# Kernel optimization log

Hardware: AMD Instinct MI355X
Metric: run time of the kernel (lower is better)

## Reference

```python
import jax, jax.numpy as jnp
import numpy as np

B, S, D = 32, 576, 768
G = 24  # sqrt(S)
TEMP = 0.01


def grid_sample_bilinear_zeros(img, grid):
    # img: (B,C,H,W), grid: (B,Hg,Wg,2) in [-1,1]; torch F.grid_sample,
    # mode='bilinear', padding_mode='zeros', align_corners=False
    Bn, C, H, W = img.shape
    gx, gy = grid[..., 0], grid[..., 1]
    ix = ((gx + 1.0) * W - 1.0) * 0.5
    iy = ((gy + 1.0) * H - 1.0) * 0.5
    x0 = jnp.floor(ix); y0 = jnp.floor(iy)
    x1 = x0 + 1.0;      y1 = y0 + 1.0
    wx1 = ix - x0; wx0 = 1.0 - wx1
    wy1 = iy - y0; wy0 = 1.0 - wy1

    def gather(xi, yi):
        valid = (xi >= 0) & (xi <= W - 1) & (yi >= 0) & (yi <= H - 1)
        xc = jnp.clip(xi, 0, W - 1).astype(jnp.int32)
        yc = jnp.clip(yi, 0, H - 1).astype(jnp.int32)
        vals = jax.vmap(lambda im, y, x: im[:, y, x])(img, yc, xc)  # (B,C,Hg,Wg)
        return vals * valid.astype(img.dtype)[:, None, :, :]

    return (gather(x0, y0) * (wx0 * wy0)[:, None]
            + gather(x1, y0) * (wx1 * wy0)[:, None]
            + gather(x0, y1) * (wx0 * wy1)[:, None]
            + gather(x1, y1) * (wx1 * wy1)[:, None])


def key_finder_net(h, W1, b1, W2, b2, W3, b3):
    # fc1 -> relu -> fc2 -> relu -> fc3 -> tanh
    h = jax.nn.relu(h @ W1 + b1)
    h = jax.nn.relu(h @ W2 + b2)
    return jnp.tanh(h @ W3 + b3)


def setup_inputs() -> dict:
    key = jax.random.key(0)
    ks = jax.random.split(key, 16)
    sd = 1.0 / np.sqrt(D)
    inp = {
        'x': jax.random.normal(ks[0], (B, S, D), dtype=jnp.float32),
        'indices': jax.random.randint(ks[1], (B, S), 0, S),
        'Wq': jax.random.normal(ks[2], (D, D), dtype=jnp.float32) * sd,
        'bq': jnp.zeros((D,), jnp.float32),
        'Wk': jax.random.normal(ks[3], (D, D), dtype=jnp.float32) * sd,
        'bk': jnp.zeros((D,), jnp.float32),
        'Wv': jax.random.normal(ks[4], (D, D), dtype=jnp.float32) * sd,
        'bv': jnp.zeros((D,), jnp.float32),
        'W1': jax.random.normal(ks[5], (2 * D, 60), dtype=jnp.float32) / np.sqrt(2 * D),
        'b1': jnp.zeros((60,), jnp.float32),
        'W2': jax.random.normal(ks[6], (60, 60), dtype=jnp.float32) / np.sqrt(60),
        'b2': jnp.zeros((60,), jnp.float32),
        'W3': jax.random.normal(ks[7], (60, 2), dtype=jnp.float32) / np.sqrt(60),
        'b3': jnp.zeros((2,), jnp.float32),
    }
    return inp


def reference(x, indices, Wq, bq, Wk, bk, Wv, bv, W1, b1, W2, b2, W3, b3):
    q = x @ Wq + bq  # (B,S,D)
    k = x @ Wk + bk
    v = x @ Wv + bv

    sample = key_finder_net(jnp.concatenate([q, k], axis=2), W1, b1, W2, b2, W3, b3)  # (B,S,2)
    # torch: cat((sample_x, sample_y), dim=1).reshape(B,G,G,2)
    flat = jnp.concatenate([sample[:, :, 0], sample[:, :, 1]], axis=1)  # (B,2S)
    grid = flat.reshape(B, G, G, 2)

    k_img = jnp.transpose(k, (0, 2, 1)).reshape(B, D, G, G)
    v_img = jnp.transpose(v, (0, 2, 1)).reshape(B, D, G, G)

    sk = grid_sample_bilinear_zeros(k_img, grid)  # (B,D,G,G)
    sv = grid_sample_bilinear_zeros(v_img, grid)
    sampled_key = jnp.transpose(sk.reshape(B, D, G * G), (0, 2, 1))   # (B,S,D)
    sampled_value = jnp.transpose(sv.reshape(B, D, G * G), (0, 2, 1))

    scores = jnp.sum(q * sampled_key, axis=-1)  # (B,S)
    return jax.nn.sigmoid(TEMP * scores)[..., None] * sampled_value
```

## Files before the change

kernel.cpp:

```cpp
#include <hip/hip_runtime.h>

typedef _Float16 f16;
typedef _Float16 f16x8 __attribute__((ext_vector_type(8)));
typedef _Float16 f16x4 __attribute__((ext_vector_type(4)));
typedef float f32x4 __attribute__((ext_vector_type(4)));
typedef float f32x16 __attribute__((ext_vector_type(16)));

constexpr int NB = 32, NS = 576, ND = 768, NG = 24;
constexpr int M_TOT = NB * NS;
constexpr int N_TOT = 3 * ND;

__global__ __launch_bounds__(256) void cast_w_t_kernel(const float* __restrict__ Wq,
                                                       const float* __restrict__ Wk,
                                                       const float* __restrict__ Wv,
                                                       f16* __restrict__ WT) {
  __shared__ float tile[64][65];
  int bt = blockIdx.x;
  int ntile = bt / 12, ktile = bt % 12;
  const float* src = (ntile < 12) ? Wq : ((ntile < 24) ? Wk : Wv);
  int n0 = (ntile % 12) * 64, k0 = ktile * 64;
  int cc = threadIdx.x & 63, rr = threadIdx.x >> 6;
#pragma unroll
  for (int i = 0; i < 16; i++) {
    int k = rr + i * 4;
    tile[cc][k] = src[(size_t)(k0 + k) * ND + n0 + cc];
  }
  __syncthreads();
#pragma unroll
  for (int i = 0; i < 16; i++) {
    int n = rr + i * 4;
    WT[(size_t)(ntile * 64 + n) * ND + k0 + cc] = (f16)tile[n][cc];
  }
}

__global__ __launch_bounds__(256) void wcT_kernel(const float* __restrict__ Wq,
                                                  const float* __restrict__ Wk,
                                                  const float* __restrict__ bq,
                                                  const float* __restrict__ bk,
                                                  const float* __restrict__ W1,
                                                  const float* __restrict__ b1,
                                                  f16* __restrict__ WcT_hi,
                                                  f16* __restrict__ WcT_lo,
                                                  float* __restrict__ bc) {
  if (blockIdx.x == 768) {
    int c = threadIdx.x;
    if (c < 60) {
      float acc = b1[c];
      for (int j = 0; j < ND; j++)
        acc += bq[j] * W1[j * 60 + c] + bk[j] * W1[(ND + j) * 60 + c];
      bc[c] = acc;
    }
    return;
  }
  __shared__ float part[4][64];
  int r = blockIdx.x;
  int wave = threadIdx.x >> 6, lane = threadIdx.x & 63;
  int c = (lane < 60) ? lane : 59;
  const float* wq = Wq + (size_t)r * ND;
  const float* wk = Wk + (size_t)r * ND;
  float acc = 0.f;
  int j0 = wave * 192;
  for (int j = j0; j < j0 + 192; j++)
    acc += wq[j] * W1[j * 60 + c] + wk[j] * W1[(ND + j) * 60 + c];
  part[wave][lane] = acc;
  __syncthreads();
  if (wave == 0 && lane < 60) {
    float v = part[0][lane] + part[1][lane] + part[2][lane] + part[3][lane];
    f16 hi = (f16)v;
    WcT_hi[(size_t)lane * ND + r] = hi;
    WcT_lo[(size_t)lane * ND + r] = (f16)(v - (float)hi);
  }
}

__global__ __launch_bounds__(256) void z1_fused_kernel(const float* __restrict__ x,
                                                       const f16* __restrict__ WcT_hi,
                                                       const f16* __restrict__ WcT_lo,
                                                       const float* __restrict__ bc,
                                                       const float* __restrict__ W2,
                                                       const float* __restrict__ b2,
                                                       const float* __restrict__ W3,
                                                       const float* __restrict__ b3,
                                                       f16* __restrict__ xb,
                                                       float* __restrict__ coords) {
  __shared__ float red[3][16][64];
  __shared__ float htile[16][60];
  int wave = threadIdx.x >> 6, lane = threadIdx.x & 63;
  int q = lane >> 4, r16 = lane & 15;
  int m0 = blockIdx.x * 16;
  int k0 = wave * 192;
  const float* xr = x + (size_t)(m0 + r16) * ND + k0;
  f16* xbr = xb + (size_t)(m0 + r16) * ND + k0;

  f32x4 acc[4];
#pragma unroll
  for (int nf = 0; nf < 4; nf++) acc[nf] = 0.f;

  for (int kk = 0; kk < 192; kk += 32) {
    int ko = kk + q * 8;
    float4 v0 = *(const float4*)(xr + ko);
    float4 v1 = *(const float4*)(xr + ko + 4);
    f16x8 a_hi, a_lo;
    float xv[8] = {v0.x, v0.y, v0.z, v0.w, v1.x, v1.y, v1.z, v1.w};
#pragma unroll
    for (int j = 0; j < 8; j++) {
      f16 h = (f16)xv[j];
      a_hi[j] = h;
      a_lo[j] = (f16)(xv[j] - (float)h);
    }
    *(f16x8*)(xbr + ko) = a_hi;
    f16x8 b_hi[4], b_lo[4];
#pragma unroll
    for (int nf = 0; nf < 4; nf++) {
      size_t off = (size_t)(nf * 16 + r16) * ND + k0 + ko;
      b_hi[nf] = *(const f16x8*)(WcT_hi + off);
      b_lo[nf] = *(const f16x8*)(WcT_lo + off);
    }
#pragma unroll
    for (int nf = 0; nf < 4; nf++) {
      acc[nf] = __builtin_amdgcn_mfma_f32_16x16x32_f16(a_hi, b_hi[nf], acc[nf], 0, 0, 0);
      acc[nf] = __builtin_amdgcn_mfma_f32_16x16x32_f16(a_lo, b_hi[nf], acc[nf], 0, 0, 0);
      acc[nf] = __builtin_amdgcn_mfma_f32_16x16x32_f16(a_hi, b_lo[nf], acc[nf], 0, 0, 0);
    }
  }

  if (wave > 0) {
#pragma unroll
    for (int nf = 0; nf < 4; nf++)
#pragma unroll
      for (int r = 0; r < 4; r++) red[wave - 1][nf * 4 + r][lane] = acc[nf][r];
  }
  __syncthreads();
  if (wave == 0) {
#pragma unroll
    for (int nf = 0; nf < 4; nf++) {
      int col = nf * 16 + r16;
      if (col < 60) {
        float bcv = bc[col];
#pragma unroll
        for (int r = 0; r < 4; r++) {
          float v = acc[nf][r] + red[0][nf * 4 + r][lane] + red[1][nf * 4 + r][lane]
                  + red[2][nf * 4 + r][lane] + bcv;
          htile[q * 4 + r][col] = fmaxf(v, 0.f);
        }
      }
    }
  }
  __syncthreads();

  int c = (lane < 60) ? lane : 59;
  float b2v = b2[c];
  float w30 = W3[c * 2 + 0], w31 = W3[c * 2 + 1];
#pragma unroll
  for (int rr = 0; rr < 4; rr++) {
    int row = wave * 4 + rr;
    float acc2 = b2v;
    for (int j = 0; j < 60; j++) acc2 = fmaf(htile[row][j], W2[j * 60 + c], acc2);
    float h2 = fmaxf(acc2, 0.f);
    float p0 = (lane < 60) ? h2 * w30 : 0.f;
    float p1 = (lane < 60) ? h2 * w31 : 0.f;
#pragma unroll
    for (int o = 32; o > 0; o >>= 1) { p0 += __shfl_down(p0, o); p1 += __shfl_down(p1, o); }
    if (lane == 0) {
      float s0 = tanhf(p0 + b3[0]);
      float s1 = tanhf(p1 + b3[1]);
      int m = m0 + row;
      int b = m / NS, s = m % NS;
      float* cb = coords + (size_t)b * (2 * NS);
      cb[(s >> 1) * 2 + (s & 1)] = s0;
      cb[(288 + (s >> 1)) * 2 + (s & 1)] = s1;
    }
  }
}

__device__ __forceinline__ void async_copy16(const f16* g, f16* l) {
  __builtin_amdgcn_global_load_lds((const __attribute__((address_space(1))) void*)g,
                                   (__attribute__((address_space(3))) void*)l, 16, 0, 0);
}

__global__ __launch_bounds__(512, 2) void gemm_kernel(const f16* __restrict__ A,
                                                      const f16* __restrict__ Bt,
                                                      const float* __restrict__ bq,
                                                      const float* __restrict__ bk,
                                                      const float* __restrict__ bv,
                                                      f16* __restrict__ C) {
  constexpr int BM = 256, BN = 256, BK = 64;
  constexpr int NKT = ND / BK;
  __shared__ __align__(16) f16 sA[2][BM * BK];
  __shared__ __align__(16) f16 sB[2][BN * BK];

  int tid = threadIdx.x;
  int lane = tid & 63, wave = tid >> 6;
  int wm = wave >> 2, wn = wave & 3;
  int orig = blockIdx.x;
  int wg = (orig & 7) * 81 + (orig >> 3);
  int bm = wg / 9, bn = wg % 9;
  int m0 = bm * BM, n0 = bn * BN;
  int r16 = lane & 15, q = lane >> 4;

  int srow = tid >> 3;
  int schunk = (tid & 7) ^ (srow & 7);
  const f16* gA = A + (size_t)(m0 + srow) * ND + schunk * 8;
  const f16* gB = Bt + (size_t)(n0 + srow) * ND + schunk * 8;

  auto stage_pair = [&](int buf, int kt, int j) {
    async_copy16(gA + (size_t)j * 64 * ND + kt * 64, &sA[buf][j * 4096 + tid * 8]);
    async_copy16(gB + (size_t)j * 64 * ND + kt * 64, &sB[buf][j * 4096 + tid * 8]);
  };

  f32x4 acc[8][4];
#pragma unroll
  for (int mi = 0; mi < 8; mi++)
#pragma unroll
    for (int ni = 0; ni < 4; ni++) acc[mi][ni] = 0.f;

#pragma unroll
  for (int j = 0; j < 4; j++) stage_pair(0, 0, j);
  asm volatile("s_waitcnt vmcnt(0)" ::: "memory");
  asm volatile("s_barrier" ::: "memory");

  for (int t = 0; t < NKT; t++) {
    int cur = t & 1;
    const f16* pA = sA[cur];
    const f16* pB = sB[cur];
    bool pf = (t + 1 < NKT);

    f16x8 bF[4][2];
#pragma unroll
    for (int ni = 0; ni < 4; ni++) {
      int R = wn * 64 + ni * 16 + r16;
#pragma unroll
      for (int s = 0; s < 2; s++) {
        int ch = (s * 4 + q) ^ (R & 7);
        bF[ni][s] = *(const f16x8*)(pB + R * 64 + ch * 8);
      }
    }

#pragma unroll
    for (int p = 0; p < 4; p++) {
      f16x8 aF[2][2];
#pragma unroll
      for (int mm = 0; mm < 2; mm++) {
        int R = wm * 128 + (p * 2 + mm) * 16 + r16;
#pragma unroll
        for (int s = 0; s < 2; s++) {
          int ch = (s * 4 + q) ^ (R & 7);
          aF[mm][s] = *(const f16x8*)(pA + R * 64 + ch * 8);
        }
      }
      if (pf) stage_pair(cur ^ 1, t + 1, p);
      asm volatile("s_barrier" ::: "memory");
      __builtin_amdgcn_sched_barrier(0);
      __builtin_amdgcn_s_setprio(1);
#pragma unroll
      for (int mm = 0; mm < 2; mm++)
#pragma unroll
        for (int ni = 0; ni < 4; ni++) {
          acc[p * 2 + mm][ni] =
              __builtin_amdgcn_mfma_f32_16x16x32_f16(bF[ni][0], aF[mm][0], acc[p * 2 + mm][ni], 0, 0, 0);
          acc[p * 2 + mm][ni] =
              __builtin_amdgcn_mfma_f32_16x16x32_f16(bF[ni][1], aF[mm][1], acc[p * 2 + mm][ni], 0, 0, 0);
        }
      __builtin_amdgcn_s_setprio(0);
      asm volatile("s_barrier" ::: "memory");
    }
    if (pf) asm volatile("s_waitcnt vmcnt(0)" ::: "memory");
    asm volatile("s_barrier" ::: "memory");
  }

  int m0g = m0 + wm * 128 + r16;
  int n0g = n0 + wn * 64 + q * 4;
#pragma unroll
  for (int mi = 0; mi < 8; mi++) {
    int gm = m0g + mi * 16;
#pragma unroll
    for (int ni = 0; ni < 4; ni++) {
      int gn = n0g + ni * 16;
      const float* bp = (gn < ND) ? (bq + gn)
                      : ((gn < 2 * ND) ? (bk + gn - ND) : (bv + gn - 2 * ND));
      float4 bias = *(const float4*)bp;
      f16x4 o;
      o[0] = (f16)(acc[mi][ni][0] + bias.x);
      o[1] = (f16)(acc[mi][ni][1] + bias.y);
      o[2] = (f16)(acc[mi][ni][2] + bias.z);
      o[3] = (f16)(acc[mi][ni][3] + bias.w);
      *(f16x4*)(C + (size_t)gm * N_TOT + gn) = o;
    }
  }
}

__global__ __launch_bounds__(256) void sample_kernel(const f16* __restrict__ qkv,
                                                     const float* __restrict__ coords,
                                                     float* __restrict__ out) {
  int wave = threadIdx.x >> 6, t = threadIdx.x & 63;
  int x8 = blockIdx.x & 7;
  int i = blockIdx.x >> 3;
  int b = x8 * 4 + (i / 144);
  int p = (i % 144) * 4 + wave;

  float gx = coords[(size_t)b * (2 * NS) + p * 2 + 0];
  float gy = coords[(size_t)b * (2 * NS) + p * 2 + 1];
  float ix = ((gx + 1.f) * (float)NG - 1.f) * 0.5f;
  float iy = ((gy + 1.f) * (float)NG - 1.f) * 0.5f;
  float x0f = floorf(ix), y0f = floorf(iy);
  float wx1 = ix - x0f, wx0 = 1.f - wx1;
  float wy1 = iy - y0f, wy0 = 1.f - wy1;
  int x0 = (int)x0f, y0 = (int)y0f, x1 = x0 + 1, y1 = y0 + 1;
  bool vx0 = (x0 >= 0) & (x0 <= NG - 1), vx1 = (x1 >= 0) & (x1 <= NG - 1);
  bool vy0 = (y0 >= 0) & (y0 <= NG - 1), vy1 = (y1 >= 0) & (y1 <= NG - 1);
  int cx0 = min(max(x0, 0), NG - 1), cx1 = min(max(x1, 0), NG - 1);
  int cy0 = min(max(y0, 0), NG - 1), cy1 = min(max(y1, 0), NG - 1);
  float w00 = wx0 * wy0 * ((vx0 && vy0) ? 1.f : 0.f);
  float w10 = wx1 * wy0 * ((vx1 && vy0) ? 1.f : 0.f);
  float w01 = wx0 * wy1 * ((vx0 && vy1) ? 1.f : 0.f);
  float w11 = wx1 * wy1 * ((vx1 && vy1) ? 1.f : 0.f);

  size_t base = (size_t)b * NS;
  const f16* r00 = qkv + (base + cy0 * NG + cx0) * N_TOT;
  const f16* r10 = qkv + (base + cy0 * NG + cx1) * N_TOT;
  const f16* r01 = qkv + (base + cy1 * NG + cx0) * N_TOT;
  const f16* r11 = qkv + (base + cy1 * NG + cx1) * N_TOT;
  const f16* qr  = qkv + (base + p) * N_TOT;

  int d0 = t * 12;
  float partial = 0.f;
  float outv[12];
#pragma unroll
  for (int ch = 0; ch < 3; ch++) {
    int d = d0 + ch * 4;
    f16x4 k00 = *(const f16x4*)(r00 + ND + d);
    f16x4 k10 = *(const f16x4*)(r10 + ND + d);
    f16x4 k01 = *(const f16x4*)(r01 + ND + d);
    f16x4 k11 = *(const f16x4*)(r11 + ND + d);
    f16x4 v00 = *(const f16x4*)(r00 + 2 * ND + d);
    f16x4 v10 = *(const f16x4*)(r10 + 2 * ND + d);
    f16x4 v01 = *(const f16x4*)(r01 + 2 * ND + d);
    f16x4 v11 = *(const f16x4*)(r11 + 2 * ND + d);
    f16x4 qv  = *(const f16x4*)(qr + d);
#pragma unroll
    for (int j = 0; j < 4; j++) {
      float sk = w00 * (float)k00[j] + w10 * (float)k10[j]
               + w01 * (float)k01[j] + w11 * (float)k11[j];
      float sv = w00 * (float)v00[j] + w10 * (float)v10[j]
               + w01 * (float)v01[j] + w11 * (float)v11[j];
      partial = fmaf((float)qv[j], sk, partial);
      outv[ch * 4 + j] = sv;
    }
  }
#pragma unroll
  for (int o = 32; o > 0; o >>= 1) partial += __shfl_down(partial, o);
  float score = __shfl(partial, 0);
  float sig = 1.f / (1.f + expf(-0.01f * score));
  float* orow = out + (size_t)(base + p) * ND;
#pragma unroll
  for (int ch = 0; ch < 3; ch++) {
    float4 st;
    st.x = sig * outv[ch * 4 + 0]; st.y = sig * outv[ch * 4 + 1];
    st.z = sig * outv[ch * 4 + 2]; st.w = sig * outv[ch * 4 + 3];
    *(float4*)(orow + d0 + ch * 4) = st;
  }
}

extern "C" void kernel_launch(void* const* d_in, const int* in_sizes, int n_in,
                              void* d_out, int out_size, void* d_ws, size_t ws_size,
                              hipStream_t stream) {
  const float* x  = (const float*)d_in[0];
  const float* Wq = (const float*)d_in[2];
  const float* bq = (const float*)d_in[3];
  const float* Wk = (const float*)d_in[4];
  const float* bk = (const float*)d_in[5];
  const float* Wv = (const float*)d_in[6];
  const float* bv = (const float*)d_in[7];
  const float* W1 = (const float*)d_in[8];
  const float* b1 = (const float*)d_in[9];
  const float* W2 = (const float*)d_in[10];
  const float* b2 = (const float*)d_in[11];
  const float* W3 = (const float*)d_in[12];
  const float* b3 = (const float*)d_in[13];
  float* out = (float*)d_out;

  char* ws = (char*)d_ws;
  f16*   xb     = (f16*)(ws);
  f16*   WT     = (f16*)(ws + 28311552);
  f16*   qkv    = (f16*)(ws + 31850496);
  f16*   WcT_hi = (f16*)(ws + 31850496);
  f16*   WcT_lo = (f16*)(ws + 31948800);
  float* bc     = (float*)(ws + 116969472);
  float* coords = (float*)(ws + 121393408);

  cast_w_t_kernel<<<dim3(432), dim3(256), 0, stream>>>(Wq, Wk, Wv, WT);
  wcT_kernel<<<dim3(769), dim3(256), 0, stream>>>(Wq, Wk, bq, bk, W1, b1, WcT_hi, WcT_lo, bc);
  z1_fused_kernel<<<dim3(M_TOT / 16), dim3(256), 0, stream>>>(x, WcT_hi, WcT_lo, bc,
                                                              W2, b2, W3, b3, xb, coords);
  gemm_kernel<<<dim3((M_TOT / 256) * (N_TOT / 256)), dim3(512), 0, stream>>>(xb, WT, bq, bk, bv, qkv);
  sample_kernel<<<dim3(M_TOT / 4), dim3(256), 0, stream>>>(qkv, coords, out);
  (void)in_sizes; (void)n_in; (void)out_size; (void)ws_size;
}
```

Before: 349.0 us.

## Merge prep kernels, deepen GEMM prefetch, coalesce sample-kernel channel access

The two weight-prep kernels become one launch, with the bias block now split across waves and reduced. The GEMM k-loop moves from a single-stage prefetch issued every sub-step to a two-tile-ahead pipeline: A and B tiles are staged separately after barriers and waited on with partial vmcnt. MFMA work is regrouped into 4x2 fragment quadrants so B fragments are reused across two sub-steps. The sample kernel now uses a strided channel mapping (ch*256 + t*4) so adjacent lanes touch adjacent memory, in exchange for trickier barrier and waitcnt correctness.

```diff
diff --git a/kernel.cpp b/kernel.cpp
--- a/kernel.cpp
+++ b/kernel.cpp
@@ -10,56 +10,57 @@
 constexpr int M_TOT = NB * NS;
 constexpr int N_TOT = 3 * ND;
 
-__global__ __launch_bounds__(256) void cast_w_t_kernel(const float* __restrict__ Wq,
-                                                       const float* __restrict__ Wk,
-                                                       const float* __restrict__ Wv,
-                                                       f16* __restrict__ WT) {
-  __shared__ float tile[64][65];
-  int bt = blockIdx.x;
-  int ntile = bt / 12, ktile = bt % 12;
-  const float* src = (ntile < 12) ? Wq : ((ntile < 24) ? Wk : Wv);
-  int n0 = (ntile % 12) * 64, k0 = ktile * 64;
-  int cc = threadIdx.x & 63, rr = threadIdx.x >> 6;
-#pragma unroll
-  for (int i = 0; i < 16; i++) {
-    int k = rr + i * 4;
-    tile[cc][k] = src[(size_t)(k0 + k) * ND + n0 + cc];
-  }
-  __syncthreads();
-#pragma unroll
-  for (int i = 0; i < 16; i++) {
-    int n = rr + i * 4;
-    WT[(size_t)(ntile * 64 + n) * ND + k0 + cc] = (f16)tile[n][cc];
-  }
-}
-
-__global__ __launch_bounds__(256) void wcT_kernel(const float* __restrict__ Wq,
-                                                  const float* __restrict__ Wk,
-                                                  const float* __restrict__ bq,
-                                                  const float* __restrict__ bk,
-                                                  const float* __restrict__ W1,
-                                                  const float* __restrict__ b1,
-                                                  f16* __restrict__ WcT_hi,
-                                                  f16* __restrict__ WcT_lo,
-                                                  float* __restrict__ bc) {
-  if (blockIdx.x == 768) {
-    int c = threadIdx.x;
-    if (c < 60) {
-      float acc = b1[c];
-      for (int j = 0; j < ND; j++)
-        acc += bq[j] * W1[j * 60 + c] + bk[j] * W1[(ND + j) * 60 + c];
-      bc[c] = acc;
+__global__ __launch_bounds__(256) void prep_kernel(const float* __restrict__ Wq,
+                                                   const float* __restrict__ Wk,
+                                                   const float* __restrict__ Wv,
+                                                   const float* __restrict__ bq,
+                                                   const float* __restrict__ bk,
+                                                   const float* __restrict__ W1,
+                                                   const float* __restrict__ b1,
+                                                   f16* __restrict__ WT,
+                                                   f16* __restrict__ WcT_hi,
+                                                   f16* __restrict__ WcT_lo,
+                                                   float* __restrict__ bc) {
+  __shared__ __align__(16) float smem[64 * 65];
+  if (blockIdx.x < 432) {
+    float (*tile)[65] = (float(*)[65])smem;
+    int bt = blockIdx.x;
+    int ntile = bt / 12, ktile = bt % 12;
+    const float* src = (ntile < 12) ? Wq : ((ntile < 24) ? Wk : Wv);
+    int n0 = (ntile % 12) * 64, k0 = ktile * 64;
+    int cc = threadIdx.x & 63, rr = threadIdx.x >> 6;
+#pragma unroll
+    for (int i = 0; i < 16; i++) {
+      int k = rr + i * 4;
+      tile[cc][k] = src[(size_t)(k0 + k) * ND + n0 + cc];
+    }
+    __syncthreads();
+#pragma unroll
+    for (int i = 0; i < 16; i++) {
+      int n = rr + i * 4;
+      WT[(size_t)(ntile * 64 + n) * ND + k0 + cc] = (f16)tile[n][cc];
     }
     return;
   }
-  __shared__ float part[4][64];
-  int r = blockIdx.x;
+  float (*part)[64] = (float(*)[64])smem;
+  int blk = blockIdx.x - 432;
   int wave = threadIdx.x >> 6, lane = threadIdx.x & 63;
   int c = (lane < 60) ? lane : 59;
+  int j0 = wave * 192;
+  if (blk == 768) {
+    float acc = 0.f;
+    for (int j = j0; j < j0 + 192; j++)
+      acc += bq[j] * W1[j * 60 + c] + bk[j] * W1[(ND + j) * 60 + c];
+    part[wave][lane] = acc;
+    __syncthreads();
+    if (wave == 0 && lane < 60)
+      bc[lane] = b1[lane] + part[0][lane] + part[1][lane] + part[2][lane] + part[3][lane];
+    return;
+  }
+  int r = blk;
   const float* wq = Wq + (size_t)r * ND;
   const float* wk = Wk + (size_t)r * ND;
   float acc = 0.f;
-  int j0 = wave * 192;
   for (int j = j0; j < j0 + 192; j++)
     acc += wq[j] * W1[j * 60 + c] + wk[j] * W1[(ND + j) * 60 + c];
   part[wave][lane] = acc;
@@ -183,10 +184,10 @@
                                                       const float* __restrict__ bk,
                                                       const float* __restrict__ bv,
                                                       f16* __restrict__ C) {
-  constexpr int BM = 256, BN = 256, BK = 64;
+  constexpr int BM = 256, BK = 64;
   constexpr int NKT = ND / BK;
   __shared__ __align__(16) f16 sA[2][BM * BK];
-  __shared__ __align__(16) f16 sB[2][BN * BK];
+  __shared__ __align__(16) f16 sB[2][BM * BK];
 
   int tid = threadIdx.x;
   int lane = tid & 63, wave = tid >> 6;
@@ -194,7 +195,7 @@
   int orig = blockIdx.x;
   int wg = (orig & 7) * 81 + (orig >> 3);
   int bm = wg / 9, bn = wg % 9;
-  int m0 = bm * BM, n0 = bn * BN;
+  int m0 = bm * BM, n0 = bn * BM;
   int r16 = lane & 15, q = lane >> 4;
 
   int srow = tid >> 3;
@@ -202,10 +203,14 @@
   const f16* gA = A + (size_t)(m0 + srow) * ND + schunk * 8;
   const f16* gB = Bt + (size_t)(n0 + srow) * ND + schunk * 8;
 
-  auto stage_pair = [&](int buf, int kt, int j) {
-    async_copy16(gA + (size_t)j * 64 * ND + kt * 64, &sA[buf][j * 4096 + tid * 8]);
-    async_copy16(gB + (size_t)j * 64 * ND + kt * 64, &sB[buf][j * 4096 + tid * 8]);
+  auto stageA = [&](int buf, int kt, int h) {
+    async_copy16(gA + (size_t)(2 * h) * 64 * ND + kt * 64, &sA[buf][(2 * h) * 4096 + tid * 8]);
+    async_copy16(gA + (size_t)(2 * h + 1) * 64 * ND + kt * 64, &sA[buf][(2 * h + 1) * 4096 + tid * 8]);
   };
+  auto stageB = [&](int buf, int kt, int h) {
+    async_copy16(gB + (size_t)(2 * h) * 64 * ND + kt * 64, &sB[buf][(2 * h) * 4096 + tid * 8]);
+    async_copy16(gB + (size_t)(2 * h + 1) * 64 * ND + kt * 64, &sB[buf][(2 * h + 1) * 4096 + tid * 8]);
+  };
 
   f32x4 acc[8][4];
 #pragma unroll
@@ -213,58 +218,59 @@
 #pragma unroll
     for (int ni = 0; ni < 4; ni++) acc[mi][ni] = 0.f;
 
-#pragma unroll
-  for (int j = 0; j < 4; j++) stage_pair(0, 0, j);
-  asm volatile("s_waitcnt vmcnt(0)" ::: "memory");
+  stageA(0, 0, 0); stageA(0, 0, 1); stageB(0, 0, 0); stageB(0, 0, 1);
+  stageA(1, 1, 0); stageA(1, 1, 1); stageB(1, 1, 0); stageB(1, 1, 1);
+  asm volatile("s_waitcnt vmcnt(8)" ::: "memory");
   asm volatile("s_barrier" ::: "memory");
 
-  for (int t = 0; t < NKT; t++) {
+  for (int t = 0; t < NKT; ++t) {
     int cur = t & 1;
     const f16* pA = sA[cur];
     const f16* pB = sB[cur];
-    bool pf = (t + 1 < NKT);
-
-    f16x8 bF[4][2];
-#pragma unroll
-    for (int ni = 0; ni < 4; ni++) {
-      int R = wn * 64 + ni * 16 + r16;
-#pragma unroll
-      for (int s = 0; s < 2; s++) {
-        int ch = (s * 4 + q) ^ (R & 7);
-        bF[ni][s] = *(const f16x8*)(pB + R * 64 + ch * 8);
+    f16x8 bF[2][2];
+#pragma unroll
+    for (int p = 0; p < 4; ++p) {
+      int a = p & 1, b = p >> 1;
+      f16x8 aF[4][2];
+#pragma unroll
+      for (int mf = 0; mf < 4; ++mf)
+#pragma unroll
+        for (int ks = 0; ks < 2; ++ks) {
+          int R = wm * 128 + a * 64 + mf * 16 + r16;
+          aF[mf][ks] = *(const f16x8*)(pA + R * 64 + (((ks * 4 + q) ^ (R & 7)) * 8));
+        }
+      if ((p & 1) == 0) {
+#pragma unroll
+        for (int nf = 0; nf < 2; ++nf)
+#pragma unroll
+          for (int ks = 0; ks < 2; ++ks) {
+            int R = wn * 64 + b * 32 + nf * 16 + r16;
+            bF[nf][ks] = *(const f16x8*)(pB + R * 64 + (((ks * 4 + q) ^ (R & 7)) * 8));
+          }
       }
-    }
-
-#pragma unroll
-    for (int p = 0; p < 4; p++) {
-      f16x8 aF[2][2];
-#pragma unroll
-      for (int mm = 0; mm < 2; mm++) {
-        int R = wm * 128 + (p * 2 + mm) * 16 + r16;
-#pragma unroll
-        for (int s = 0; s < 2; s++) {
-          int ch = (s * 4 + q) ^ (R & 7);
-          aF[mm][s] = *(const f16x8*)(pA + R * 64 + ch * 8);
-        }
-      }
-      if (pf) stage_pair(cur ^ 1, t + 1, p);
+      if (p >= 2)
+        asm volatile("s_waitcnt lgkmcnt(0)" ::: "memory");
       asm volatile("s_barrier" ::: "memory");
+      if (p == 2 && t + 2 < NKT) { stageB(cur, t + 2, 0); stageB(cur, t + 2, 1); }
+      if (p == 3 && t + 2 < NKT) { stageA(cur, t + 2, 0); stageA(cur, t + 2, 1); }
       __builtin_amdgcn_sched_barrier(0);
       __builtin_amdgcn_s_setprio(1);
 #pragma unroll
-      for (int mm = 0; mm < 2; mm++)
-#pragma unroll
-        for (int ni = 0; ni < 4; ni++) {
-          acc[p * 2 + mm][ni] =
-              __builtin_amdgcn_mfma_f32_16x16x32_f16(bF[ni][0], aF[mm][0], acc[p * 2 + mm][ni], 0, 0, 0);
-          acc[p * 2 + mm][ni] =
-              __builtin_amdgcn_mfma_f32_16x16x32_f16(bF[ni][1], aF[mm][1], acc[p * 2 + mm][ni], 0, 0, 0);
+      for (int mf = 0; mf < 4; ++mf)
+#pragma unroll
+        for (int nf = 0; nf < 2; ++nf) {
+          f32x4 v = acc[a * 4 + mf][b * 2 + nf];
+          v = __builtin_amdgcn_mfma_f32_16x16x32_f16(bF[nf][0], aF[mf][0], v, 0, 0, 0);
+          v = __builtin_amdgcn_mfma_f32_16x16x32_f16(bF[nf][1], aF[mf][1], v, 0, 0, 0);
+          acc[a * 4 + mf][b * 2 + nf] = v;
         }
       __builtin_amdgcn_s_setprio(0);
+      if (p == 3) {
+        if (t < NKT - 2)       asm volatile("s_waitcnt vmcnt(8)" ::: "memory");
+        else if (t == NKT - 2) asm volatile("s_waitcnt vmcnt(0)" ::: "memory");
+      }
       asm volatile("s_barrier" ::: "memory");
     }
-    if (pf) asm volatile("s_waitcnt vmcnt(0)" ::: "memory");
-    asm volatile("s_barrier" ::: "memory");
   }
 
   int m0g = m0 + wm * 128 + r16;
@@ -321,12 +327,11 @@
   const f16* r11 = qkv + (base + cy1 * NG + cx1) * N_TOT;
   const f16* qr  = qkv + (base + p) * N_TOT;
 
-  int d0 = t * 12;
   float partial = 0.f;
   float outv[12];
 #pragma unroll
   for (int ch = 0; ch < 3; ch++) {
-    int d = d0 + ch * 4;
+    int d = ch * 256 + t * 4;
     f16x4 k00 = *(const f16x4*)(r00 + ND + d);
     f16x4 k10 = *(const f16x4*)(r10 + ND + d);
     f16x4 k01 = *(const f16x4*)(r01 + ND + d);
@@ -353,10 +358,11 @@
   float* orow = out + (size_t)(base + p) * ND;
 #pragma unroll
   for (int ch = 0; ch < 3; ch++) {
+    int d = ch * 256 + t * 4;
     float4 st;
     st.x = sig * outv[ch * 4 + 0]; st.y = sig * outv[ch * 4 + 1];
     st.z = sig * outv[ch * 4 + 2]; st.w = sig * outv[ch * 4 + 3];
-    *(float4*)(orow + d0 + ch * 4) = st;
+    *(float4*)(orow + d) = st;
   }
 }
 
@@ -387,8 +393,8 @@
   float* bc     = (float*)(ws + 116969472);
   float* coords = (float*)(ws + 121393408);
 
-  cast_w_t_kernel<<<dim3(432), dim3(256), 0, stream>>>(Wq, Wk, Wv, WT);
-  wcT_kernel<<<dim3(769), dim3(256), 0, stream>>>(Wq, Wk, bq, bk, W1, b1, WcT_hi, WcT_lo, bc);
+  prep_kernel<<<dim3(432 + 769), dim3(256), 0, stream>>>(Wq, Wk, Wv, bq, bk, W1, b1,
+                                                         WT, WcT_hi, WcT_lo, bc);
   z1_fused_kernel<<<dim3(M_TOT / 16), dim3(256), 0, stream>>>(x, WcT_hi, WcT_lo, bc,
                                                               W2, b2, W3, b3, xb, coords);
   gemm_kernel<<<dim3((M_TOT / 256) * (N_TOT / 256)), dim3(512), 0, stream>>>(xb, WT, bq, bk, bv, qkv);
```

Measured after the change: 337.1 us. -3.4%, faster.
